# Performance work log

Hardware: AMD Instinct MI355X
Metric: run time of the kernel (lower is better)

Reference implementation:

```python
import jax, jax.numpy as jnp
import numpy as np


def _pointnet(x, w1, b1, w2, b2, w3, b3):
    # x: [B, 3, P]; shared per-point MLP 3->64->128->128, max-pool over points -> [B,128]
    h = jax.nn.relu(jnp.einsum('oc,bcp->bop', w1, x) + b1[None, :, None])
    h = jax.nn.relu(jnp.einsum('oc,bcp->bop', w2, h) + b2[None, :, None])
    h = jax.nn.relu(jnp.einsum('oc,bcp->bop', w3, h) + b3[None, :, None])
    return h.max(axis=2)


def _lstm_layer(x, wih, whh, b):
    # x: [B, T, D]; standard LSTM (pytorch gate order i,f,g,o), returns [B, T, 128]
    B = x.shape[0]
    h0 = jnp.zeros((B, 128), x.dtype)
    def step(carry, xt):
        h, c = carry
        g = xt @ wih.T + h @ whh.T + b
        i, f, gg, o = jnp.split(g, 4, axis=-1)
        c = jax.nn.sigmoid(f) * c + jax.nn.sigmoid(i) * jnp.tanh(gg)
        h = jax.nn.sigmoid(o) * jnp.tanh(c)
        return (h, c), h
    _, hs = jax.lax.scan(step, (h0, h0), jnp.swapaxes(x, 0, 1))
    return jnp.swapaxes(hs, 0, 1)


def _edgeconv(x, aff, tw, tb, pw, pb, N):
    # DGL EdgeConv, max aggregation. Edges: det i -> track (N+j) where aff[i,j]==1, plus
    # self loops on every node. Message on edge u->v: theta(x_u - x_v) + phi(x_v).
    phi = x @ pw.T + pb                                   # [N+M, 256]
    diff = x[:N][:, None, :] - x[N:][None, :, :]          # [N, M, 256] (x_src - x_dst)
    msg = jnp.einsum('nmc,oc->nmo', diff, tw) + tb        # theta applied to diffs
    msg = jnp.where(aff[:, :, None] > 0, msg, jnp.finfo(x.dtype).min)
    h_trk = phi[N:] + jnp.maximum(tb, msg.max(axis=0))    # self-loop message is theta(0)=tb
    h_det = phi[:N] + tb                                  # dets only receive their self loop
    return jnp.concatenate([h_det, h_trk], axis=0)


def _forward(det_pc_in_box, det_boxes3d, track_pc_in_box, track_boxes3d, init_aff_matrix,
             pn_w1, pn_b1, pn_w2, pn_b2, pn_w3, pn_b3,
             mlp_w1, mlp_b1, mlp_w2, mlp_b2,
             l0_wih, l0_whh, l0_b, l1_wih, l1_whh, l1_b,
             ec_tw, ec_tb, ec_pw, ec_pb,
             er_w1, er_b1, er_w2, er_b2):
    N = det_pc_in_box.shape[0]
    det_app = _pointnet(jnp.swapaxes(det_pc_in_box, 1, 2), pn_w1, pn_b1, pn_w2, pn_b2, pn_w3, pn_b3)
    trk_app = _pointnet(jnp.swapaxes(track_pc_in_box, 1, 2), pn_w1, pn_b1, pn_w2, pn_b2, pn_w3, pn_b3)
    det_mot = jax.nn.relu(det_boxes3d @ mlp_w1.T + mlp_b1) @ mlp_w2.T + mlp_b2
    trk_mot = _lstm_layer(_lstm_layer(track_boxes3d, l0_wih, l0_whh, l0_b), l1_wih, l1_whh, l1_b)[:, -1, :]
    h = jnp.concatenate([jnp.concatenate([det_app, det_mot], axis=1),
                         jnp.concatenate([trk_app, trk_mot], axis=1)], axis=0)  # [N+M, 256]
    for k in range(4):
        h = jax.nn.relu(_edgeconv(h, init_aff_matrix, ec_tw[k], ec_tb[k], ec_pw[k], ec_pb[k], N))
    # pairwise affinity: (track - det) differences through small MLP + sigmoid (BCE head)
    edges = h[N:][None, :, :] - h[:N][:, None, :]                                # [N, M, 256]
    e = jax.nn.relu(jnp.einsum('nmc,oc->nmo', edges, er_w1) + er_b1)             # [N, M, 64]
    regr = jax.nn.sigmoid(jnp.einsum('nmo,ko->nmk', e, er_w2) + er_b2)[..., 0]   # [N, M]
    valid = init_aff_matrix * regr
    valid = jnp.where(valid == 0, jnp.asarray(99.0, valid.dtype), valid)
    return valid


def setup_inputs() -> dict:
    key = jax.random.key(0)
    ks = jax.random.split(key, 20)
    N, M, P, T = 512, 512, 256, 10
    f = jnp.float32
    def rn(k, shp):
        return jax.random.normal(k, shp, dtype=f) * 0.05
    return {
        'det_pc_in_box': jax.random.normal(ks[0], (N, P, 3), dtype=f),
        'det_boxes3d': jax.random.normal(ks[1], (N, 9), dtype=f),
        'track_pc_in_box': jax.random.normal(ks[2], (M, P, 3), dtype=f),
        'track_boxes3d': jax.random.normal(ks[3], (M, T, 9), dtype=f),
        'init_aff_matrix': jnp.ones((N, M), dtype=f),
        'gt_affinity_matrix': jnp.zeros((N, M), dtype=jnp.int32),
        'pn_w1': rn(ks[4], (64, 3)), 'pn_b1': jnp.zeros((64,), f),
        'pn_w2': rn(ks[5], (128, 64)), 'pn_b2': jnp.zeros((128,), f),
        'pn_w3': rn(ks[6], (128, 128)), 'pn_b3': jnp.zeros((128,), f),
        'mlp_w1': rn(ks[7], (64, 9)), 'mlp_b1': jnp.zeros((64,), f),
        'mlp_w2': rn(ks[8], (128, 64)), 'mlp_b2': jnp.zeros((128,), f),
        'l0_wih': rn(ks[9], (512, 9)), 'l0_whh': rn(ks[10], (512, 128)), 'l0_b': jnp.zeros((512,), f),
        'l1_wih': rn(ks[11], (512, 128)), 'l1_whh': rn(ks[12], (512, 128)), 'l1_b': jnp.zeros((512,), f),
        'ec_tw': rn(ks[13], (4, 256, 256)), 'ec_tb': jnp.zeros((4, 256), f),
        'ec_pw': rn(ks[14], (4, 256, 256)), 'ec_pb': jnp.zeros((4, 256), f),
        'er_w1': rn(ks[15], (64, 256)), 'er_b1': jnp.zeros((64,), f),
        'er_w2': rn(ks[16], (1, 64)), 'er_b2': jnp.zeros((1,), f),
    }


def reference(det_pc_in_box, det_boxes3d, track_pc_in_box, track_boxes3d, init_aff_matrix,
              gt_affinity_matrix,
              pn_w1, pn_b1, pn_w2, pn_b2, pn_w3, pn_b3,
              mlp_w1, mlp_b1, mlp_w2, mlp_b2,
              l0_wih, l0_whh, l0_b, l1_wih, l1_whh, l1_b,
              ec_tw, ec_tb, ec_pw, ec_pb,
              er_w1, er_b1, er_w2, er_b2):
    # gt_affinity_matrix is only used by the training loss; inference path ignores it.
    return _forward(det_pc_in_box, det_boxes3d, track_pc_in_box, track_boxes3d, init_aff_matrix,
                    pn_w1, pn_b1, pn_w2, pn_b2, pn_w3, pn_b3,
                    mlp_w1, mlp_b1, mlp_w2, mlp_b2,
                    l0_wih, l0_whh, l0_b, l1_wih, l1_whh, l1_b,
                    ec_tw, ec_tb, ec_pw, ec_pb,
                    er_w1, er_b1, er_w2, er_b2)
```

## Files before the change

### kernel.cpp

```cpp
#include <hip/hip_runtime.h>
#include <math.h>

#define N_DET 512
#define N_TRK 512
#define NPTS  256

typedef __attribute__((ext_vector_type(8))) short short8;
typedef __attribute__((ext_vector_type(4))) float f32x4;
typedef unsigned short ushort_t;

__device__ __forceinline__ float sigm(float x) { return 1.f / (1.f + expf(-x)); }

__device__ __forceinline__ unsigned short f2bf(float f) {
    unsigned u = __float_as_uint(f);
    u += 0x7FFF + ((u >> 16) & 1);
    return (unsigned short)(u >> 16);
}
__device__ __forceinline__ float bf2f(unsigned short h) {
    return __uint_as_float(((unsigned)h) << 16);
}

__global__ __launch_bounds__(64) void pn_wprep_kernel(
    const float* __restrict__ w2, const float* __restrict__ w3,
    unsigned short* __restrict__ wfrag)
{
    const int f = blockIdx.x;
    const int lane = threadIdx.x;
    const int lm = lane & 15, lg = lane >> 4;
    const float* src;
    if (f < 16) {
        const int s = f >> 3, n = f & 7;
        src = w2 + (size_t)(n*16 + lm)*64 + s*32 + lg*8;
    } else {
        const int f2 = f - 16, s = f2 >> 3, n = f2 & 7;
        src = w3 + (size_t)(n*16 + lm)*128 + s*32 + lg*8;
    }
    short8 v;
#pragma unroll
    for (int j = 0; j < 8; ++j) v[j] = (short)f2bf(src[j]);
    *reinterpret_cast<short8*>(wfrag + ((size_t)f*64 + lane)*8) = v;
}

__global__ __launch_bounds__(64) void ec_wprep_kernel(
    const float* __restrict__ tw, const float* __restrict__ pw,
    unsigned short* __restrict__ whi, unsigned short* __restrict__ wlo)
{
    const int id = blockIdx.x;
    const int layer = id >> 8;
    const int ntile = (id >> 3) & 31, kf = id & 7;
    const int lane = threadIdx.x;
    const int lm = lane & 15, lg = lane >> 4;
    const int col = ntile*16 + lm, k = kf*32 + lg*8;
    const float* src = (col < 256)
        ? tw + ((size_t)layer*256 + col)*256 + k
        : pw + ((size_t)layer*256 + (col - 256))*256 + k;
    short8 hi, lo;
#pragma unroll
    for (int j = 0; j < 8; ++j) {
        const float f = src[j];
        const unsigned short h = f2bf(f);
        hi[j] = (short)h;
        lo[j] = (short)f2bf(f - bf2f(h));
    }
    const size_t off = ((size_t)id*64 + lane)*8;
    *reinterpret_cast<short8*>(whi + off) = hi;
    *reinterpret_cast<short8*>(wlo + off) = lo;
}

__global__ __launch_bounds__(64) void lstm_wprep_kernel(
    const float* __restrict__ whh0, const float* __restrict__ wih1,
    const float* __restrict__ whh1, unsigned short* __restrict__ wf)
{
    const int id = blockIdx.x;
    const int mat = id >> 7, rest = id & 127;
    const int nt = rest >> 2, kf = rest & 3;
    const int lane = threadIdx.x;
    const int lm = lane & 15, lg = lane >> 4;
    const float* src = (mat == 0) ? whh0 : ((mat == 1) ? wih1 : whh1);
    const float* p = src + (size_t)(nt*16 + lm)*128 + kf*32 + lg*8;
    short8 v;
#pragma unroll
    for (int j = 0; j < 8; ++j) v[j] = (short)f2bf(p[j]);
    *reinterpret_cast<short8*>(wf + ((size_t)id*64 + lane)*8) = v;
}

__global__ __launch_bounds__(512) void lstm_xg0_kernel(
    const float* __restrict__ xseq, const float* __restrict__ wih0,
    float* __restrict__ xg0)
{
    __shared__ float xs[8][12];
    const int tid = threadIdx.x;
    const int m0 = blockIdx.x * 8;
    if (tid < 72) xs[tid / 9][tid % 9] = xseq[(size_t)m0*9 + tid];
    float wx[9];
#pragma unroll
    for (int c = 0; c < 9; ++c) wx[c] = wih0[tid*9 + c];
    __syncthreads();
#pragma unroll
    for (int i = 0; i < 8; ++i) {
        float s = 0.f;
#pragma unroll
        for (int c = 0; c < 9; ++c) s = fmaf(wx[c], xs[i][c], s);
        xg0[(size_t)(m0 + i)*512 + tid] = s;
    }
}

__global__ __launch_bounds__(256) void lstm_xg1_kernel(
    const unsigned short* __restrict__ h0hi, const unsigned short* __restrict__ h0lo,
    const unsigned short* __restrict__ wfrag, float* __restrict__ xg1)
{
    const int tid = threadIdx.x, lane = tid & 63, w = tid >> 6;
    const int lm = lane & 15, lg = lane >> 4;
    const int m0 = blockIdx.x*64 + w*16;
    const int bn = blockIdx.y;
    const int arow = m0 + lm;
    short8 ahi[4], alo[4];
#pragma unroll
    for (int kf = 0; kf < 4; ++kf) {
        ahi[kf] = *reinterpret_cast<const short8*>(h0hi + (size_t)arow*128 + kf*32 + lg*8);
        alo[kf] = *reinterpret_cast<const short8*>(h0lo + (size_t)arow*128 + kf*32 + lg*8);
    }
#pragma unroll
    for (int nt = 0; nt < 4; ++nt) {
        f32x4 acc = {0.f, 0.f, 0.f, 0.f};
#pragma unroll
        for (int kf = 0; kf < 4; ++kf) {
            const short8 bf = *reinterpret_cast<const short8*>(
                wfrag + ((size_t)((bn*4 + nt)*4 + kf)*64 + lane)*8);
            acc = __builtin_amdgcn_mfma_f32_16x16x32_bf16(ahi[kf], bf, acc, 0, 0, 0);
            acc = __builtin_amdgcn_mfma_f32_16x16x32_bf16(alo[kf], bf, acc, 0, 0, 0);
        }
#pragma unroll
        for (int r = 0; r < 4; ++r)
            xg1[(size_t)(m0 + lg*4 + r)*512 + bn*64 + nt*16 + lm] = acc[r];
    }
}

template<int LAYER>
__global__ __launch_bounds__(512, 2) void lstm_mfma_kernel(
    const unsigned short* __restrict__ wfrag,
    const float* __restrict__ xg, const float* __restrict__ bias,
    unsigned short* __restrict__ h0hi, unsigned short* __restrict__ h0lo,
    float* __restrict__ hout)
{
    __shared__ unsigned short hfhi[4*64*8];
    __shared__ unsigned short hflo[4*64*8];
    __shared__ float gs[512*20];

    const int tid = threadIdx.x;
    const int lane = tid & 63, w = tid >> 6;
    const int lm = lane & 15, lg = lane >> 4;
    const int b0 = blockIdx.x * 16;

    short8 wf[4][4];
#pragma unroll
    for (int nt = 0; nt < 4; ++nt)
#pragma unroll
        for (int kf = 0; kf < 4; ++kf)
            wf[nt][kf] = *reinterpret_cast<const short8*>(
                wfrag + ((size_t)((w*4 + nt)*4 + kf)*64 + lane)*8);

    for (int i = tid; i < 2048; i += 512) { hfhi[i] = 0; hflo[i] = 0; }

    const int mj = tid & 127;
    const int mb0 = (tid >> 7) * 4;
    const float bi = bias[mj], bf_ = bias[128 + mj];
    const float bg = bias[256 + mj], bo = bias[384 + mj];
    const int hkf = mj >> 5, hlg = (mj >> 3) & 3, hjj = mj & 7;
    float c[4] = {0.f, 0.f, 0.f, 0.f};

    __syncthreads();

    for (int t = 0; t < 10; ++t) {
        float xgv[4][4];
#pragma unroll
        for (int s = 0; s < 4; ++s) {
            const size_t btg = ((size_t)(b0 + mb0 + s)*10 + t)*512;
            xgv[s][0] = xg[btg + mj];
            xgv[s][1] = xg[btg + 128 + mj];
            xgv[s][2] = xg[btg + 256 + mj];
            xgv[s][3] = xg[btg + 384 + mj];
        }
        short8 ahi[4], alo[4];
#pragma unroll
        for (int kf = 0; kf < 4; ++kf) {
            ahi[kf] = *reinterpret_cast<const short8*>(&hfhi[(kf*64 + lane)*8]);
            alo[kf] = *reinterpret_cast<const short8*>(&hflo[(kf*64 + lane)*8]);
        }
#pragma unroll
        for (int nt = 0; nt < 4; ++nt) {
            f32x4 acc = {0.f, 0.f, 0.f, 0.f};
#pragma unroll
            for (int kf = 0; kf < 4; ++kf) {
                acc = __builtin_amdgcn_mfma_f32_16x16x32_bf16(ahi[kf], wf[nt][kf], acc, 0, 0, 0);
                acc = __builtin_amdgcn_mfma_f32_16x16x32_bf16(alo[kf], wf[nt][kf], acc, 0, 0, 0);
            }
            const int g = w*64 + nt*16 + lm;
            float4 tmp; tmp.x = acc[0]; tmp.y = acc[1]; tmp.z = acc[2]; tmp.w = acc[3];
            *(float4*)&gs[g*20 + lg*4] = tmp;
        }
        __syncthreads();
#pragma unroll
        for (int s = 0; s < 4; ++s) {
            const int b = mb0 + s;
            const float gi = gs[mj*20 + b]         + xgv[s][0] + bi;
            const float gf = gs[(128 + mj)*20 + b] + xgv[s][1] + bf_;
            const float gg = gs[(256 + mj)*20 + b] + xgv[s][2] + bg;
            const float go = gs[(384 + mj)*20 + b] + xgv[s][3] + bo;
            c[s] = sigm(gf)*c[s] + sigm(gi)*tanhf(gg);
            const float hn = sigm(go)*tanhf(c[s]);
            const unsigned short hh = f2bf(hn);
            const unsigned short hl = f2bf(hn - bf2f(hh));
            hfhi[(hkf*64 + hlg*16 + b)*8 + hjj] = hh;
            hflo[(hkf*64 + hlg*16 + b)*8 + hjj] = hl;
            if constexpr (LAYER == 0) {
                h0hi[((size_t)(b0 + b)*10 + t)*128 + mj] = hh;
                h0lo[((size_t)(b0 + b)*10 + t)*128 + mj] = hl;
            } else {
                if (t == 9)
                    hout[(size_t)(N_DET + b0 + b)*256 + 128 + mj] = hn;
            }
        }
        __syncthreads();
    }
}

__global__ __launch_bounds__(256) void h2bf_kernel(
    const float* __restrict__ h,
    unsigned short* __restrict__ hi, unsigned short* __restrict__ lo)
{
    const int id = blockIdx.x * 256 + threadIdx.x;
    const float4 v = *(const float4*)(h + (size_t)id*4);
    ushort_t h4[4], l4[4];
    const float vv[4] = {v.x, v.y, v.z, v.w};
#pragma unroll
    for (int j = 0; j < 4; ++j) {
        h4[j] = f2bf(vv[j]);
        l4[j] = f2bf(vv[j] - bf2f(h4[j]));
    }
    *(ulong1*)(hi + (size_t)id*4) = *(ulong1*)h4;
    *(ulong1*)(lo + (size_t)id*4) = *(ulong1*)l4;
}

__global__ __launch_bounds__(256) void pointnet_mfma_kernel(
    const float* __restrict__ det_pc, const float* __restrict__ trk_pc,
    const float* __restrict__ w1, const float* __restrict__ b1,
    const unsigned short* __restrict__ wfrag,
    const float* __restrict__ b2, const float* __restrict__ b3,
    float* __restrict__ hout)
{
    __shared__ unsigned short h1t[4][16][72];
    __shared__ unsigned short h2t[4][16][136];
    __shared__ float wmaxs[4][128];

    const int tid = threadIdx.x;
    const int box = blockIdx.x;
    const int lane = tid & 63, w = tid >> 6;
    const int lm = lane & 15, lg = lane >> 4;

    const float* pc = (box < N_DET) ? det_pc + ((size_t)box*NPTS + tid)*3
                                    : trk_pc + ((size_t)(box - N_DET)*NPTS + tid)*3;
    const float x = pc[0], y = pc[1], z = pc[2];
    unsigned h1p[32];
#pragma unroll
    for (int j = 0; j < 32; ++j) {
        const int c0 = 2*j, c1 = 2*j + 1;
        float s0 = fmaf(w1[c0*3+0], x, fmaf(w1[c0*3+1], y, fmaf(w1[c0*3+2], z, b1[c0])));
        float s1 = fmaf(w1[c1*3+0], x, fmaf(w1[c1*3+1], y, fmaf(w1[c1*3+2], z, b1[c1])));
        h1p[j] = (unsigned)f2bf(fmaxf(s0, 0.f)) | ((unsigned)f2bf(fmaxf(s1, 0.f)) << 16);
    }

    short8 w2f[16];
#pragma unroll
    for (int f = 0; f < 16; ++f)
        w2f[f] = *reinterpret_cast<const short8*>(wfrag + ((size_t)f*64 + lane)*8);
    float b2v[8];
#pragma unroll
    for (int n = 0; n < 8; ++n) b2v[n] = b2[n*16 + lm];

    float pm[8];
#pragma unroll
    for (int n = 0; n < 8; ++n) pm[n] = -3.0e38f;

    for (int t = 0; t < 4; ++t) {
        __syncthreads();
        if (lg == t) {
#pragma unroll
            for (int q = 0; q < 8; ++q) {
                uint4 v;
                v.x = h1p[q*4+0]; v.y = h1p[q*4+1];
                v.z = h1p[q*4+2]; v.w = h1p[q*4+3];
                *(uint4*)&h1t[w][lm][q*8] = v;
            }
        }
        __syncthreads();
        const short8 a0 = *reinterpret_cast<const short8*>(&h1t[w][lm][lg*8]);
        const short8 a1 = *reinterpret_cast<const short8*>(&h1t[w][lm][32 + lg*8]);
#pragma unroll
        for (int n = 0; n < 8; ++n) {
            f32x4 acc = {0.f, 0.f, 0.f, 0.f};
            acc = __builtin_amdgcn_mfma_f32_16x16x32_bf16(a0, w2f[n],     acc, 0, 0, 0);
            acc = __builtin_amdgcn_mfma_f32_16x16x32_bf16(a1, w2f[8 + n], acc, 0, 0, 0);
#pragma unroll
            for (int r = 0; r < 4; ++r) {
                const float v = fmaxf(acc[r] + b2v[n], 0.f);
                h2t[w][lg*4 + r][n*16 + lm] = f2bf(v);
            }
        }
        __syncthreads();
        const short8 c0 = *reinterpret_cast<const short8*>(&h2t[w][lm][  0 + lg*8]);
        const short8 c1 = *reinterpret_cast<const short8*>(&h2t[w][lm][ 32 + lg*8]);
        const short8 c2 = *reinterpret_cast<const short8*>(&h2t[w][lm][ 64 + lg*8]);
        const short8 c3 = *reinterpret_cast<const short8*>(&h2t[w][lm][ 96 + lg*8]);
#pragma unroll
        for (int n = 0; n < 8; ++n) {
            f32x4 acc = {0.f, 0.f, 0.f, 0.f};
            const short8 b0f = *reinterpret_cast<const short8*>(wfrag + ((size_t)(16 +      n)*64 + lane)*8);
            const short8 b1f = *reinterpret_cast<const short8*>(wfrag + ((size_t)(16 +  8 + n)*64 + lane)*8);
            const short8 b2f = *reinterpret_cast<const short8*>(wfrag + ((size_t)(16 + 16 + n)*64 + lane)*8);
            const short8 b3f = *reinterpret_cast<const short8*>(wfrag + ((size_t)(16 + 24 + n)*64 + lane)*8);
            acc = __builtin_amdgcn_mfma_f32_16x16x32_bf16(c0, b0f, acc, 0, 0, 0);
            acc = __builtin_amdgcn_mfma_f32_16x16x32_bf16(c1, b1f, acc, 0, 0, 0);
            acc = __builtin_amdgcn_mfma_f32_16x16x32_bf16(c2, b2f, acc, 0, 0, 0);
            acc = __builtin_amdgcn_mfma_f32_16x16x32_bf16(c3, b3f, acc, 0, 0, 0);
#pragma unroll
            for (int r = 0; r < 4; ++r) pm[n] = fmaxf(pm[n], acc[r]);
        }
    }

#pragma unroll
    for (int n = 0; n < 8; ++n) {
        float v = pm[n];
        v = fmaxf(v, __shfl_xor(v, 16, 64));
        v = fmaxf(v, __shfl_xor(v, 32, 64));
        pm[n] = v;
    }
    if (lg == 0) {
#pragma unroll
        for (int n = 0; n < 8; ++n) wmaxs[w][n*16 + lm] = pm[n];
    }
    __syncthreads();
    if (tid < 128) {
        const float m = fmaxf(fmaxf(wmaxs[0][tid], wmaxs[1][tid]),
                              fmaxf(wmaxs[2][tid], wmaxs[3][tid]));
        hout[(size_t)box*256 + tid] = fmaxf(m + b3[tid], 0.f);
    }
}

__global__ __launch_bounds__(128) void detmlp_kernel(
    const float* __restrict__ boxes,
    const float* __restrict__ w1, const float* __restrict__ b1,
    const float* __restrict__ w2, const float* __restrict__ b2,
    float* __restrict__ hout)
{
    __shared__ float xb[9];
    __shared__ float h1[64];
    const int b = blockIdx.x, t = threadIdx.x;
    if (t < 9) xb[t] = boxes[b*9 + t];
    __syncthreads();
    if (t < 64) {
        float s = b1[t];
#pragma unroll
        for (int c = 0; c < 9; ++c) s = fmaf(w1[t*9+c], xb[c], s);
        h1[t] = fmaxf(s, 0.f);
    }
    __syncthreads();
    float s = b2[t];
    const float* wr = w2 + t*64;
#pragma unroll
    for (int c = 0; c < 64; ++c) s = fmaf(wr[c], h1[c], s);
    hout[(size_t)b * 256 + 128 + t] = s;
}

__global__ __launch_bounds__(256) void ec_gemm_mfma_kernel(
    const unsigned short* __restrict__ hhi, const unsigned short* __restrict__ hlo,
    const unsigned short* __restrict__ whi, const unsigned short* __restrict__ wlo,
    const float* __restrict__ tb, const float* __restrict__ pb,
    float* __restrict__ Abuf, float* __restrict__ Bbuf,
    float* __restrict__ phiT, float* __restrict__ hnext,
    unsigned short* __restrict__ nhi, unsigned short* __restrict__ nlo)
{
    const int bm = blockIdx.x, bn = blockIdx.y;
    const int tid = threadIdx.x, lane = tid & 63, w = tid >> 6;
    const int lm = lane & 15, lg = lane >> 4;
    const int mrow0 = bm*32 + (w & 1)*16;
    const int nt0   = bn*4 + (w >> 1)*2;
    const int arow  = mrow0 + lm;

    f32x4 acc[2] = {{0.f,0.f,0.f,0.f},{0.f,0.f,0.f,0.f}};

#pragma unroll
    for (int kf = 0; kf < 8; ++kf) {
        const short8 ahi = *reinterpret_cast<const short8*>(
            hhi + (size_t)arow*256 + kf*32 + lg*8);
        const short8 alo = *reinterpret_cast<const short8*>(
            hlo + (size_t)arow*256 + kf*32 + lg*8);
#pragma unroll
        for (int n2 = 0; n2 < 2; ++n2) {
            const size_t foff = ((size_t)((nt0 + n2)*8 + kf)*64 + lane)*8;
            const short8 bhi = *reinterpret_cast<const short8*>(whi + foff);
            const short8 blo = *reinterpret_cast<const short8*>(wlo + foff);
            acc[n2] = __builtin_amdgcn_mfma_f32_16x16x32_bf16(ahi, bhi, acc[n2], 0, 0, 0);
            acc[n2] = __builtin_amdgcn_mfma_f32_16x16x32_bf16(alo, bhi, acc[n2], 0, 0, 0);
            acc[n2] = __builtin_amdgcn_mfma_f32_16x16x32_bf16(ahi, blo, acc[n2], 0, 0, 0);
        }
    }

#pragma unroll
    for (int n2 = 0; n2 < 2; ++n2) {
        const int col = (nt0 + n2)*16 + lm;
#pragma unroll
        for (int r = 0; r < 4; ++r) {
            const int row = mrow0 + lg*4 + r;
            float v = acc[n2][r];
            if (col < 256) {
                if (row < N_DET) Abuf[(size_t)row*256 + col] = v;
                else             Bbuf[(size_t)(row - N_DET)*256 + col] = v;
            } else {
                const int o = col - 256;
                v += pb[o];
                if (row < N_DET) {
                    const float hv = fmaxf(v + tb[o], 0.f);
                    hnext[(size_t)row*256 + o] = hv;
                    const unsigned short hb = f2bf(hv);
                    nhi[(size_t)row*256 + o] = hb;
                    nlo[(size_t)row*256 + o] = f2bf(hv - bf2f(hb));
                } else {
                    phiT[(size_t)(row - N_DET)*256 + o] = v;
                }
            }
        }
    }
}

#define CM_MT 16
#define CM_OT 32
#define CM_NC 64

__global__ __launch_bounds__(256) void ec_colmax_kernel(
    const float* __restrict__ aff,
    const float* __restrict__ Abuf, const float* __restrict__ Bbuf,
    const float* __restrict__ phiT, const float* __restrict__ tb,
    float* __restrict__ hnext,
    unsigned short* __restrict__ nhi, unsigned short* __restrict__ nlo)
{
    __shared__ float As[CM_NC][CM_OT + 4];
    __shared__ float Fs[CM_NC][CM_MT + 4];
    const int t = threadIdx.x;
    const int mtile = blockIdx.x;
    const int otile = blockIdx.y;
    const int mi = t >> 4, oi = t & 15;

    float mx0 = -3.0e38f, mx1 = -3.0e38f;

    for (int n0 = 0; n0 < 512; n0 += CM_NC) {
        if (n0) __syncthreads();
        {
            const int r = t >> 3, c4 = (t & 7) * 4;
#pragma unroll
            for (int rr = 0; rr < 2; ++rr) {
                const float4 v = *(const float4*)(
                    Abuf + (size_t)(n0 + rr*32 + r)*256 + otile*CM_OT + c4);
                *(float4*)&As[rr*32 + r][c4] = v;
            }
        }
        {
            const int n = t >> 2, m4 = (t & 3) * 4;
            const float4 a = *(const float4*)(
                aff + (size_t)(n0 + n)*512 + mtile*CM_MT + m4);
            float4 f;
            f.x = (a.x > 0.f) ? 0.f : -3.0e38f;
            f.y = (a.y > 0.f) ? 0.f : -3.0e38f;
            f.z = (a.z > 0.f) ? 0.f : -3.0e38f;
            f.w = (a.w > 0.f) ? 0.f : -3.0e38f;
            *(float4*)&Fs[n][m4] = f;
        }
        __syncthreads();
#pragma unroll 4
        for (int n = 0; n < CM_NC; ++n) {
            const float f = Fs[n][mi];
            const float2 a = *(const float2*)&As[n][oi*2];
            mx0 = fmaxf(mx0, a.x + f);
            mx1 = fmaxf(mx1, a.y + f);
        }
    }

    const int m = mtile*CM_MT + mi;
    const int o = otile*CM_OT + oi*2;
    const float2 tb2 = *(const float2*)(tb + o);
    const float2 bb  = *(const float2*)(Bbuf + (size_t)m*256 + o);
    const float2 ph  = *(const float2*)(phiT + (size_t)m*256 + o);
    const float v0 = fmaxf(tb2.x, mx0 - bb.x + tb2.x);
    const float v1 = fmaxf(tb2.y, mx1 - bb.y + tb2.y);
    float2 outv;
    outv.x = fmaxf(ph.x + v0, 0.f);
    outv.y = fmaxf(ph.y + v1, 0.f);
    const size_t base = (size_t)(N_DET + m)*256 + o;
    *(float2*)(hnext + base) = outv;
    const unsigned short h0 = f2bf(outv.x), h1 = f2bf(outv.y);
    nhi[base]     = h0;
    nhi[base + 1] = h1;
    nlo[base]     = f2bf(outv.x - bf2f(h0));
    nlo[base + 1] = f2bf(outv.y - bf2f(h1));
}

__global__ __launch_bounds__(256) void headp_kernel(
    const float* __restrict__ h, const float* __restrict__ w1, float* __restrict__ P)
{
    const int tid = threadIdx.x;
    const int o = tid & 63, rl = tid >> 6;
    const int row = blockIdx.x * 4 + rl;
    const float* hr = h + (size_t)row * 256;
    const float* wr = w1 + (size_t)o * 256;
    float s0 = 0.f, s1 = 0.f, s2 = 0.f, s3 = 0.f;
#pragma unroll
    for (int c = 0; c < 256; c += 4) {
        const float4 hv = *(const float4*)(hr + c);
        const float4 wv = *(const float4*)(wr + c);
        s0 = fmaf(hv.x, wv.x, s0);
        s1 = fmaf(hv.y, wv.y, s1);
        s2 = fmaf(hv.z, wv.z, s2);
        s3 = fmaf(hv.w, wv.w, s3);
    }
    P[(size_t)row * 64 + o] = (s0 + s1) + (s2 + s3);
}

__global__ __launch_bounds__(256) void pairwise_kernel(
    const float* __restrict__ P, const float* __restrict__ aff,
    const float* __restrict__ eb1, const float* __restrict__ ew2, const float* __restrict__ eb2,
    float* __restrict__ out)
{
    __shared__ float pd[64], sb1[64], sw2[64];
    const int n = blockIdx.y;
    const int t = threadIdx.x;
    if (t < 64)       pd[t]        = P[(size_t)n * 64 + t];
    else if (t < 128) sb1[t - 64]  = eb1[t - 64];
    else if (t < 192) sw2[t - 128] = ew2[t - 128];
    __syncthreads();
    const int m = blockIdx.x * 256 + t;
    const float* pt = P + (size_t)(N_DET + m) * 64;
    float s = eb2[0];
#pragma unroll
    for (int c = 0; c < 64; c += 4) {
        const float4 pv = *(const float4*)(pt + c);
        float e;
        e = fmaxf(pv.x - pd[c+0] + sb1[c+0], 0.f); s = fmaf(e, sw2[c+0], s);
        e = fmaxf(pv.y - pd[c+1] + sb1[c+1], 0.f); s = fmaf(e, sw2[c+1], s);
        e = fmaxf(pv.z - pd[c+2] + sb1[c+2], 0.f); s = fmaf(e, sw2[c+2], s);
        e = fmaxf(pv.w - pd[c+3] + sb1[c+3], 0.f); s = fmaf(e, sw2[c+3], s);
    }
    const float r = 1.f / (1.f + expf(-s));
    const float v = aff[(size_t)n * 512 + m] * r;
    out[(size_t)n * 512 + m] = (v == 0.f) ? 99.f : v;
}

extern "C" void kernel_launch(void* const* d_in, const int* in_sizes, int n_in,
                              void* d_out, int out_size, void* d_ws, size_t ws_size,
                              hipStream_t stream)
{
    (void)in_sizes; (void)n_in; (void)out_size; (void)ws_size;

    const float* det_pc  = (const float*)d_in[0];
    const float* det_box = (const float*)d_in[1];
    const float* trk_pc  = (const float*)d_in[2];
    const float* trk_box = (const float*)d_in[3];
    const float* aff     = (const float*)d_in[4];
    const float* pn_w1  = (const float*)d_in[6];
    const float* pn_b1  = (const float*)d_in[7];
    const float* pn_w2  = (const float*)d_in[8];
    const float* pn_b2  = (const float*)d_in[9];
    const float* pn_w3  = (const float*)d_in[10];
    const float* pn_b3  = (const float*)d_in[11];
    const float* mlp_w1 = (const float*)d_in[12];
    const float* mlp_b1 = (const float*)d_in[13];
    const float* mlp_w2 = (const float*)d_in[14];
    const float* mlp_b2 = (const float*)d_in[15];
    const float* l0_wih = (const float*)d_in[16];
    const float* l0_whh = (const float*)d_in[17];
    const float* l0_b   = (const float*)d_in[18];
    const float* l1_wih = (const float*)d_in[19];
    const float* l1_whh = (const float*)d_in[20];
    const float* l1_b   = (const float*)d_in[21];
    const float* ec_tw  = (const float*)d_in[22];
    const float* ec_tb  = (const float*)d_in[23];
    const float* ec_pw  = (const float*)d_in[24];
    const float* ec_pb  = (const float*)d_in[25];
    const float* er_w1  = (const float*)d_in[26];
    const float* er_b1  = (const float*)d_in[27];
    const float* er_w2  = (const float*)d_in[28];
    const float* er_b2  = (const float*)d_in[29];

    float* ws    = (float*)d_ws;
    float* hA    = ws;
    float* hB    = hA + 1024*256;
    float* Abuf  = hB + 1024*256;
    float* Bbuf  = Abuf + 512*256;
    float* phiT  = Bbuf + 512*256;
    float* P     = phiT + 512*256;
    float* xg0   = P + 1024*64;
    float* xg1   = xg0 + 5120*512;
    unsigned short* wfrag  = (unsigned short*)(xg1 + 5120*512);
    unsigned short* ecwhi  = wfrag + 48*64*8;
    unsigned short* ecwlo  = ecwhi + 1024*64*8;
    unsigned short* lstmwf = ecwlo + 1024*64*8;
    unsigned short* h0hi   = lstmwf + 3*128*64*8;
    unsigned short* h0lo   = h0hi + 5120*128;
    unsigned short* hbfA_hi = h0lo + 5120*128;
    unsigned short* hbfA_lo = hbfA_hi + 1024*256;
    unsigned short* hbfB_hi = hbfA_lo + 1024*256;
    unsigned short* hbfB_lo = hbfB_hi + 1024*256;

    pn_wprep_kernel<<<48, 64, 0, stream>>>(pn_w2, pn_w3, wfrag);
    ec_wprep_kernel<<<1024, 64, 0, stream>>>(ec_tw, ec_pw, ecwhi, ecwlo);
    lstm_wprep_kernel<<<384, 64, 0, stream>>>(l0_whh, l1_wih, l1_whh, lstmwf);
    pointnet_mfma_kernel<<<1024, 256, 0, stream>>>(det_pc, trk_pc, pn_w1, pn_b1,
                                                   wfrag, pn_b2, pn_b3, hA);
    detmlp_kernel<<<512, 128, 0, stream>>>(det_box, mlp_w1, mlp_b1, mlp_w2, mlp_b2, hA);

    lstm_xg0_kernel<<<640, 512, 0, stream>>>(trk_box, l0_wih, xg0);
    lstm_mfma_kernel<0><<<32, 512, 0, stream>>>(lstmwf, xg0, l0_b, h0hi, h0lo, nullptr);
    lstm_xg1_kernel<<<dim3(80, 8), 256, 0, stream>>>(h0hi, h0lo, lstmwf + 128*64*8, xg1);
    lstm_mfma_kernel<1><<<32, 512, 0, stream>>>(lstmwf + 2*128*64*8, xg1, l1_b,
                                                nullptr, nullptr, hA);

    h2bf_kernel<<<256, 256, 0, stream>>>(hA, hbfA_hi, hbfA_lo);

    float* hcur = hA;  float* hnext = hB;
    unsigned short* chi = hbfA_hi; unsigned short* clo = hbfA_lo;
    unsigned short* nhi = hbfB_hi; unsigned short* nlo = hbfB_lo;
    for (int k = 0; k < 4; ++k) {
        const float* tb = ec_tb + (size_t)k * 256;
        const float* pb = ec_pb + (size_t)k * 256;
        ec_gemm_mfma_kernel<<<dim3(32, 8), 256, 0, stream>>>(
            chi, clo, ecwhi + (size_t)k*256*64*8, ecwlo + (size_t)k*256*64*8,
            tb, pb, Abuf, Bbuf, phiT, hnext, nhi, nlo);
        ec_colmax_kernel<<<dim3(32, 8), 256, 0, stream>>>(aff, Abuf, Bbuf, phiT, tb,
                                                          hnext, nhi, nlo);
        float* tf = hcur; hcur = hnext; hnext = tf;
        unsigned short* th = chi; chi = nhi; nhi = th;
        unsigned short* tl = clo; clo = nlo; nlo = tl;
    }

    headp_kernel<<<256, 256, 0, stream>>>(hcur, er_w1, P);
    pairwise_kernel<<<dim3(2, 512), 256, 0, stream>>>(P, aff, er_b1, er_w2, er_b2,
                                                      (float*)d_out);
}
```

Before: 349.3 us.

## Merge weight-prep kernels, fuse LSTM layer-0 input projection and bf16 splitting

Combines the three weight-preparation kernels into one launch. The layer-0 LSTM input projection (9-wide) now runs inside the recurrent kernel from staged inputs in shared memory, which drops the separate xg0 kernel and its global buffer. The hi/lo bf16 split of the hidden state is produced directly by pointnet, detmlp and the LSTM output, removing the h2bf kernel. Fewer launches and less global traffic, at the cost of extra registers and FMA work in the serial LSTM loop. The launch-bounds occupancy hint of 2 is also dropped.

```diff
diff --git a/kernel.cpp b/kernel.cpp
--- a/kernel.cpp
+++ b/kernel.cpp
@@ -20,88 +20,62 @@
     return __uint_as_float(((unsigned)h) << 16);
 }
 
-__global__ __launch_bounds__(64) void pn_wprep_kernel(
-    const float* __restrict__ w2, const float* __restrict__ w3,
-    unsigned short* __restrict__ wfrag)
-{
-    const int f = blockIdx.x;
+__global__ __launch_bounds__(64) void wprep_all_kernel(
+    const float* __restrict__ pnw2, const float* __restrict__ pnw3,
+    const float* __restrict__ ectw, const float* __restrict__ ecpw,
+    const float* __restrict__ whh0, const float* __restrict__ wih1,
+    const float* __restrict__ whh1,
+    unsigned short* __restrict__ wfrag,
+    unsigned short* __restrict__ ecwhi, unsigned short* __restrict__ ecwlo,
+    unsigned short* __restrict__ lstmwf)
+{
+    const int bid = blockIdx.x;
     const int lane = threadIdx.x;
     const int lm = lane & 15, lg = lane >> 4;
-    const float* src;
-    if (f < 16) {
-        const int s = f >> 3, n = f & 7;
-        src = w2 + (size_t)(n*16 + lm)*64 + s*32 + lg*8;
+
+    if (bid < 48) {
+        const int f = bid;
+        const float* src;
+        if (f < 16) {
+            const int s = f >> 3, n = f & 7;
+            src = pnw2 + (size_t)(n*16 + lm)*64 + s*32 + lg*8;
+        } else {
+            const int f2 = f - 16, s = f2 >> 3, n = f2 & 7;
+            src = pnw3 + (size_t)(n*16 + lm)*128 + s*32 + lg*8;
+        }
+        short8 v;
+#pragma unroll
+        for (int j = 0; j < 8; ++j) v[j] = (short)f2bf(src[j]);
+        *reinterpret_cast<short8*>(wfrag + ((size_t)f*64 + lane)*8) = v;
+    } else if (bid < 48 + 1024) {
+        const int id = bid - 48;
+        const int layer = id >> 8;
+        const int ntile = (id >> 3) & 31, kf = id & 7;
+        const int col = ntile*16 + lm, k = kf*32 + lg*8;
+        const float* src = (col < 256)
+            ? ectw + ((size_t)layer*256 + col)*256 + k
+            : ecpw + ((size_t)layer*256 + (col - 256))*256 + k;
+        short8 hi, lo;
+#pragma unroll
+        for (int j = 0; j < 8; ++j) {
+            const float f = src[j];
+            const unsigned short h = f2bf(f);
+            hi[j] = (short)h;
+            lo[j] = (short)f2bf(f - bf2f(h));
+        }
+        const size_t off = ((size_t)id*64 + lane)*8;
+        *reinterpret_cast<short8*>(ecwhi + off) = hi;
+        *reinterpret_cast<short8*>(ecwlo + off) = lo;
     } else {
-        const int f2 = f - 16, s = f2 >> 3, n = f2 & 7;
-        src = w3 + (size_t)(n*16 + lm)*128 + s*32 + lg*8;
-    }
-    short8 v;
-#pragma unroll
-    for (int j = 0; j < 8; ++j) v[j] = (short)f2bf(src[j]);
-    *reinterpret_cast<short8*>(wfrag + ((size_t)f*64 + lane)*8) = v;
-}
-
-__global__ __launch_bounds__(64) void ec_wprep_kernel(
-    const float* __restrict__ tw, const float* __restrict__ pw,
-    unsigned short* __restrict__ whi, unsigned short* __restrict__ wlo)
-{
-    const int id = blockIdx.x;
-    const int layer = id >> 8;
-    const int ntile = (id >> 3) & 31, kf = id & 7;
-    const int lane = threadIdx.x;
-    const int lm = lane & 15, lg = lane >> 4;
-    const int col = ntile*16 + lm, k = kf*32 + lg*8;
-    const float* src = (col < 256)
-        ? tw + ((size_t)layer*256 + col)*256 + k
-        : pw + ((size_t)layer*256 + (col - 256))*256 + k;
-    short8 hi, lo;
-#pragma unroll
-    for (int j = 0; j < 8; ++j) {
-        const float f = src[j];
-        const unsigned short h = f2bf(f);
-        hi[j] = (short)h;
-        lo[j] = (short)f2bf(f - bf2f(h));
-    }
-    const size_t off = ((size_t)id*64 + lane)*8;
-    *reinterpret_cast<short8*>(whi + off) = hi;
-    *reinterpret_cast<short8*>(wlo + off) = lo;
-}
-
-__global__ __launch_bounds__(64) void lstm_wprep_kernel(
-    const float* __restrict__ whh0, const float* __restrict__ wih1,
-    const float* __restrict__ whh1, unsigned short* __restrict__ wf)
-{
-    const int id = blockIdx.x;
-    const int mat = id >> 7, rest = id & 127;
-    const int nt = rest >> 2, kf = rest & 3;
-    const int lane = threadIdx.x;
-    const int lm = lane & 15, lg = lane >> 4;
-    const float* src = (mat == 0) ? whh0 : ((mat == 1) ? wih1 : whh1);
-    const float* p = src + (size_t)(nt*16 + lm)*128 + kf*32 + lg*8;
-    short8 v;
-#pragma unroll
-    for (int j = 0; j < 8; ++j) v[j] = (short)f2bf(p[j]);
-    *reinterpret_cast<short8*>(wf + ((size_t)id*64 + lane)*8) = v;
-}
-
-__global__ __launch_bounds__(512) void lstm_xg0_kernel(
-    const float* __restrict__ xseq, const float* __restrict__ wih0,
-    float* __restrict__ xg0)
-{
-    __shared__ float xs[8][12];
-    const int tid = threadIdx.x;
-    const int m0 = blockIdx.x * 8;
-    if (tid < 72) xs[tid / 9][tid % 9] = xseq[(size_t)m0*9 + tid];
-    float wx[9];
-#pragma unroll
-    for (int c = 0; c < 9; ++c) wx[c] = wih0[tid*9 + c];
-    __syncthreads();
-#pragma unroll
-    for (int i = 0; i < 8; ++i) {
-        float s = 0.f;
-#pragma unroll
-        for (int c = 0; c < 9; ++c) s = fmaf(wx[c], xs[i][c], s);
-        xg0[(size_t)(m0 + i)*512 + tid] = s;
+        const int id = bid - 1072;
+        const int mat = id >> 7, rest = id & 127;
+        const int nt = rest >> 2, kf = rest & 3;
+        const float* src = (mat == 0) ? whh0 : ((mat == 1) ? wih1 : whh1);
+        const float* p = src + (size_t)(nt*16 + lm)*128 + kf*32 + lg*8;
+        short8 v;
+#pragma unroll
+        for (int j = 0; j < 8; ++j) v[j] = (short)f2bf(p[j]);
+        *reinterpret_cast<short8*>(lstmwf + ((size_t)id*64 + lane)*8) = v;
     }
 }
 
@@ -137,15 +111,19 @@
 }
 
 template<int LAYER>
-__global__ __launch_bounds__(512, 2) void lstm_mfma_kernel(
+__global__ __launch_bounds__(512) void lstm_mfma_kernel(
     const unsigned short* __restrict__ wfrag,
-    const float* __restrict__ xg, const float* __restrict__ bias,
+    const float* __restrict__ xg_or_xseq,
+    const float* __restrict__ wih0,
+    const float* __restrict__ bias,
     unsigned short* __restrict__ h0hi, unsigned short* __restrict__ h0lo,
-    float* __restrict__ hout)
+    float* __restrict__ hout,
+    unsigned short* __restrict__ nhi, unsigned short* __restrict__ nlo)
 {
     __shared__ unsigned short hfhi[4*64*8];
     __shared__ unsigned short hflo[4*64*8];
     __shared__ float gs[512*20];
+    __shared__ float xstage[16*10*9];
 
     const int tid = threadIdx.x;
     const int lane = tid & 63, w = tid >> 6;
@@ -169,17 +147,42 @@
     const int hkf = mj >> 5, hlg = (mj >> 3) & 3, hjj = mj & 7;
     float c[4] = {0.f, 0.f, 0.f, 0.f};
 
+    float wx[4][9];
+    if constexpr (LAYER == 0) {
+        for (int i = tid; i < 1440; i += 512)
+            xstage[i] = xg_or_xseq[(size_t)b0*90 + i];
+#pragma unroll
+        for (int q = 0; q < 4; ++q)
+#pragma unroll
+            for (int cc = 0; cc < 9; ++cc)
+                wx[q][cc] = wih0[(size_t)(q*128 + mj)*9 + cc];
+    }
+
     __syncthreads();
 
     for (int t = 0; t < 10; ++t) {
         float xgv[4][4];
-#pragma unroll
-        for (int s = 0; s < 4; ++s) {
-            const size_t btg = ((size_t)(b0 + mb0 + s)*10 + t)*512;
-            xgv[s][0] = xg[btg + mj];
-            xgv[s][1] = xg[btg + 128 + mj];
-            xgv[s][2] = xg[btg + 256 + mj];
-            xgv[s][3] = xg[btg + 384 + mj];
+        if constexpr (LAYER == 0) {
+#pragma unroll
+            for (int s = 0; s < 4; ++s) {
+                const float* xr = &xstage[(mb0 + s)*90 + t*9];
+#pragma unroll
+                for (int q = 0; q < 4; ++q) {
+                    float acc = 0.f;
+#pragma unroll
+                    for (int cc = 0; cc < 9; ++cc) acc = fmaf(wx[q][cc], xr[cc], acc);
+                    xgv[s][q] = acc;
+                }
+            }
+        } else {
+#pragma unroll
+            for (int s = 0; s < 4; ++s) {
+                const size_t btg = ((size_t)(b0 + mb0 + s)*10 + t)*512;
+                xgv[s][0] = xg_or_xseq[btg + mj];
+                xgv[s][1] = xg_or_xseq[btg + 128 + mj];
+                xgv[s][2] = xg_or_xseq[btg + 256 + mj];
+                xgv[s][3] = xg_or_xseq[btg + 384 + mj];
+            }
         }
         short8 ahi[4], alo[4];
 #pragma unroll
@@ -217,29 +220,16 @@
                 h0hi[((size_t)(b0 + b)*10 + t)*128 + mj] = hh;
                 h0lo[((size_t)(b0 + b)*10 + t)*128 + mj] = hl;
             } else {
-                if (t == 9)
-                    hout[(size_t)(N_DET + b0 + b)*256 + 128 + mj] = hn;
+                if (t == 9) {
+                    const size_t base = (size_t)(N_DET + b0 + b)*256 + 128 + mj;
+                    hout[base] = hn;
+                    nhi[base] = hh;
+                    nlo[base] = hl;
+                }
             }
         }
         __syncthreads();
     }
-}
-
-__global__ __launch_bounds__(256) void h2bf_kernel(
-    const float* __restrict__ h,
-    unsigned short* __restrict__ hi, unsigned short* __restrict__ lo)
-{
-    const int id = blockIdx.x * 256 + threadIdx.x;
-    const float4 v = *(const float4*)(h + (size_t)id*4);
-    ushort_t h4[4], l4[4];
-    const float vv[4] = {v.x, v.y, v.z, v.w};
-#pragma unroll
-    for (int j = 0; j < 4; ++j) {
-        h4[j] = f2bf(vv[j]);
-        l4[j] = f2bf(vv[j] - bf2f(h4[j]));
-    }
-    *(ulong1*)(hi + (size_t)id*4) = *(ulong1*)h4;
-    *(ulong1*)(lo + (size_t)id*4) = *(ulong1*)l4;
 }
 
 __global__ __launch_bounds__(256) void pointnet_mfma_kernel(
@@ -247,7 +237,8 @@
     const float* __restrict__ w1, const float* __restrict__ b1,
     const unsigned short* __restrict__ wfrag,
     const float* __restrict__ b2, const float* __restrict__ b3,
-    float* __restrict__ hout)
+    float* __restrict__ hout,
+    unsigned short* __restrict__ nhi, unsigned short* __restrict__ nlo)
 {
     __shared__ unsigned short h1t[4][16][72];
     __shared__ unsigned short h2t[4][16][136];
@@ -343,7 +334,12 @@
     if (tid < 128) {
         const float m = fmaxf(fmaxf(wmaxs[0][tid], wmaxs[1][tid]),
                               fmaxf(wmaxs[2][tid], wmaxs[3][tid]));
-        hout[(size_t)box*256 + tid] = fmaxf(m + b3[tid], 0.f);
+        const float v = fmaxf(m + b3[tid], 0.f);
+        const size_t base = (size_t)box*256 + tid;
+        hout[base] = v;
+        const unsigned short hh = f2bf(v);
+        nhi[base] = hh;
+        nlo[base] = f2bf(v - bf2f(hh));
     }
 }
 
@@ -351,7 +347,8 @@
     const float* __restrict__ boxes,
     const float* __restrict__ w1, const float* __restrict__ b1,
     const float* __restrict__ w2, const float* __restrict__ b2,
-    float* __restrict__ hout)
+    float* __restrict__ hout,
+    unsigned short* __restrict__ nhi, unsigned short* __restrict__ nlo)
 {
     __shared__ float xb[9];
     __shared__ float h1[64];
@@ -369,7 +366,11 @@
     const float* wr = w2 + t*64;
 #pragma unroll
     for (int c = 0; c < 64; ++c) s = fmaf(wr[c], h1[c], s);
-    hout[(size_t)b * 256 + 128 + t] = s;
+    const size_t base = (size_t)b * 256 + 128 + t;
+    hout[base] = s;
+    const unsigned short hh = f2bf(s);
+    nhi[base] = hh;
+    nlo[base] = f2bf(s - bf2f(hh));
 }
 
 __global__ __launch_bounds__(256) void ec_gemm_mfma_kernel(
@@ -597,8 +598,7 @@
     float* Bbuf  = Abuf + 512*256;
     float* phiT  = Bbuf + 512*256;
     float* P     = phiT + 512*256;
-    float* xg0   = P + 1024*64;
-    float* xg1   = xg0 + 5120*512;
+    float* xg1   = P + 1024*64;
     unsigned short* wfrag  = (unsigned short*)(xg1 + 5120*512);
     unsigned short* ecwhi  = wfrag + 48*64*8;
     unsigned short* ecwlo  = ecwhi + 1024*64*8;
@@ -610,20 +610,20 @@
     unsigned short* hbfB_hi = hbfA_lo + 1024*256;
     unsigned short* hbfB_lo = hbfB_hi + 1024*256;
 
-    pn_wprep_kernel<<<48, 64, 0, stream>>>(pn_w2, pn_w3, wfrag);
-    ec_wprep_kernel<<<1024, 64, 0, stream>>>(ec_tw, ec_pw, ecwhi, ecwlo);
-    lstm_wprep_kernel<<<384, 64, 0, stream>>>(l0_whh, l1_wih, l1_whh, lstmwf);
+    wprep_all_kernel<<<1456, 64, 0, stream>>>(pn_w2, pn_w3, ec_tw, ec_pw,
+                                              l0_whh, l1_wih, l1_whh,
+                                              wfrag, ecwhi, ecwlo, lstmwf);
     pointnet_mfma_kernel<<<1024, 256, 0, stream>>>(det_pc, trk_pc, pn_w1, pn_b1,
-                                                   wfrag, pn_b2, pn_b3, hA);
-    detmlp_kernel<<<512, 128, 0, stream>>>(det_box, mlp_w1, mlp_b1, mlp_w2, mlp_b2, hA);
-
-    lstm_xg0_kernel<<<640, 512, 0, stream>>>(trk_box, l0_wih, xg0);
-    lstm_mfma_kernel<0><<<32, 512, 0, stream>>>(lstmwf, xg0, l0_b, h0hi, h0lo, nullptr);
+                                                   wfrag, pn_b2, pn_b3, hA,
+                                                   hbfA_hi, hbfA_lo);
+    detmlp_kernel<<<512, 128, 0, stream>>>(det_box, mlp_w1, mlp_b1, mlp_w2, mlp_b2,
+                                           hA, hbfA_hi, hbfA_lo);
+
+    lstm_mfma_kernel<0><<<32, 512, 0, stream>>>(lstmwf, trk_box, l0_wih, l0_b,
+                                                h0hi, h0lo, nullptr, nullptr, nullptr);
     lstm_xg1_kernel<<<dim3(80, 8), 256, 0, stream>>>(h0hi, h0lo, lstmwf + 128*64*8, xg1);
-    lstm_mfma_kernel<1><<<32, 512, 0, stream>>>(lstmwf + 2*128*64*8, xg1, l1_b,
-                                                nullptr, nullptr, hA);
-
-    h2bf_kernel<<<256, 256, 0, stream>>>(hA, hbfA_hi, hbfA_lo);
+    lstm_mfma_kernel<1><<<32, 512, 0, stream>>>(lstmwf + 2*128*64*8, xg1, nullptr, l1_b,
+                                                nullptr, nullptr, hA, hbfA_hi, hbfA_lo);
 
     float* hcur = hA;  float* hnext = hB;
     unsigned short* chi = hbfA_hi; unsigned short* clo = hbfA_lo;
```

Measured after the change: 341.4 us. 2.3% less time.
